# Kernel optimization log

Measured on AMD Instinct MI355X. Metric: run time of the kernel, lower is better.

## Reference

```python
import jax, jax.numpy as jnp
import numpy as np
import math

HEAD_SIZE = 64
WINDOW = 512  # sliding_window_size


def setup_inputs() -> dict:
    key = jax.random.key(0)
    k1, k2, k3, k4 = jax.random.split(key, 4)
    B, T, C = 4, 4096, 1024
    x = jax.random.normal(k1, (B, T, C), dtype=jnp.float32)
    # torch nn.Linear(C, head_size, bias=False) computes x @ W.T with W [hs, C];
    # we store the transposed [C, hs] layout so projection is x @ w.
    s = 1.0 / math.sqrt(C)
    w_key = jax.random.uniform(k2, (C, HEAD_SIZE), jnp.float32, -s, s)
    w_query = jax.random.uniform(k3, (C, HEAD_SIZE), jnp.float32, -s, s)
    w_value = jax.random.uniform(k4, (C, HEAD_SIZE), jnp.float32, -s, s)
    return {"x": x, "w_key": w_key, "w_query": w_query, "w_value": w_value}


def reference(x, w_key, w_query, w_value):
    # Non-cache path (use_cache=False): keys/values are the fresh projections,
    # q_start = k_start = 0, win_size = sliding_window_size.
    B, T, C = x.shape
    q = x @ w_query          # [B, T, hs]
    k = x @ w_key            # [B, T, hs]
    v = x @ w_value          # [B, T, hs]

    # attn_scores = q @ k^T  -> [B, T, T]
    scores = jnp.einsum('btd,bsd->bts', q, k)

    # Sliding-window causal mask: invalid where diff < 0 or diff >= window,
    # with diff = q_pos - k_pos.
    pos = jnp.arange(T)
    diff = pos[:, None] - pos[None, :]          # [T, T]
    mask_bool = (diff < 0) | (diff >= WINDOW)

    scale = math.sqrt(HEAD_SIZE)
    scores = jnp.where(mask_bool[None, :, :], -jnp.inf, scores)
    attn = jax.nn.softmax(scores / scale, axis=-1)  # dropout p=0.0 -> identity

    out = jnp.einsum('bts,bsd->btd', attn, v)   # [B, T, hs]
    return out
```

## Files before the change

kernel.cpp:

```cpp
#include <hip/hip_runtime.h>
#include <hip/hip_bf16.h>
#include <math.h>

#define BB 4
#define TT 4096
#define CC 1024
#define HS 64
#define WIN 512
#define NROW (BB*TT)

typedef float f32x4 __attribute__((ext_vector_type(4)));
typedef short bf16x8 __attribute__((ext_vector_type(8)));

#define MFMA16(a, b, c) __builtin_amdgcn_mfma_f32_16x16x32_bf16((a), (b), (c), 0, 0, 0)

#define GLOAD_LDS(gp, lp) __builtin_amdgcn_global_load_lds( \
    (const __attribute__((address_space(1))) void*)(gp), \
    (__attribute__((address_space(3))) void*)(lp), 16, 0, 0)

__device__ inline unsigned short f2b(float f) {
  union { __hip_bfloat16 h; unsigned short u; } v;
  v.h = __float2bfloat16(f);
  return v.u;
}

__global__ __launch_bounds__(256) void pack_w_kernel(
    const float* __restrict__ wq, const float* __restrict__ wk,
    const float* __restrict__ wv, unsigned short* __restrict__ wp)
{
  int t = blockIdx.x * 256 + threadIdx.x;
  int kg = t / 48;
  int nq = t % 48;
  int n0 = nq * 4;
  int m  = n0 >> 6;
  int c  = n0 & 63;
  const float* w = (m == 0) ? wq : (m == 1) ? wk : wv;
  float4 v = *(const float4*)&w[(size_t)kg * HS + c];
  int kt = kg >> 5;
  int hi = (kg >> 3) & 3;
  int j  = kg & 7;
  float vals[4] = {v.x, v.y, v.z, v.w};
  #pragma unroll
  for (int i = 0; i < 4; ++i) {
    int n  = n0 + i;
    int nb = n >> 4;
    int rl = n & 15;
    int lane = hi * 16 + rl;
    wp[((size_t)(kt * 12 + nb) * 64 + lane) * 8 + j] = f2b(vals[i]);
  }
}

__global__ __launch_bounds__(512) void proj_mfma_kernel(
    const float* __restrict__ x, const unsigned short* __restrict__ wp,
    unsigned short* __restrict__ q_ws, unsigned short* __restrict__ k_ws,
    unsigned short* __restrict__ vt_ws)
{
  __shared__ unsigned char lds[131072];
  unsigned char* const xb0 = lds;
  unsigned char* const xb1 = lds + 16384;
  unsigned char* const wb0 = lds + 32768;
  unsigned char* const wb1 = lds + 81920;

  const int tid = threadIdx.x;
  const int l   = tid & 63;
  const int wid = tid >> 6;
  const int cq  = wid & 3;
  const int rh  = wid >> 2;
  const int rl  = l & 15;
  const int hi  = l >> 4;
  const int r0  = blockIdx.x * 64;

  f32x4 acc[2][3];
  #pragma unroll
  for (int g = 0; g < 2; ++g)
    #pragma unroll
    for (int j = 0; j < 3; ++j) acc[g][j] = (f32x4){0.f, 0.f, 0.f, 0.f};

  f32x4 xr[2][2];

#define SXL(KS) { \
    _Pragma("unroll") \
    for (int it = 0; it < 2; ++it) { \
      int u = it * 512 + tid; \
      const float* gp = x + (size_t)(r0 + (u >> 4)) * CC + (KS) * 128 + (u & 15) * 8; \
      xr[it][0] = *(const f32x4*)gp; \
      xr[it][1] = *(const f32x4*)(gp + 4); \
    } }

#define XPACK(XB) { \
    _Pragma("unroll") \
    for (int it = 0; it < 2; ++it) { \
      int u = it * 512 + tid; \
      int row = u >> 4, seg = u & 15; \
      uint4 pk; \
      pk.x = (unsigned)f2b(xr[it][0][0]) | ((unsigned)f2b(xr[it][0][1]) << 16); \
      pk.y = (unsigned)f2b(xr[it][0][2]) | ((unsigned)f2b(xr[it][0][3]) << 16); \
      pk.z = (unsigned)f2b(xr[it][1][0]) | ((unsigned)f2b(xr[it][1][1]) << 16); \
      pk.w = (unsigned)f2b(xr[it][1][2]) | ((unsigned)f2b(xr[it][1][3]) << 16); \
      *(uint4*)((XB) + row * 256 + (((seg ^ (row & 7))) << 4)) = pk; \
    } }

#define SW(KS, WB) { \
    const unsigned short* wsrc = wp + (size_t)(KS) * 24576; \
    _Pragma("unroll") \
    for (int i = 0; i < 6; ++i) { \
      int s = i * 512 + tid; \
      GLOAD_LDS(wsrc + s * 8, (WB) + s * 16); \
    } }

#define COMP(XB, WB) { \
    _Pragma("unroll") \
    for (int kt = 0; kt < 4; ++kt) { \
      bf16x8 afr[2]; \
      _Pragma("unroll") \
      for (int g = 0; g < 2; ++g) { \
        int row = rh * 32 + g * 16 + rl; \
        int seg = kt * 4 + hi; \
        afr[g] = *(const bf16x8*)((XB) + row * 256 + ((seg ^ (row & 7)) << 4)); \
      } \
      _Pragma("unroll") \
      for (int j = 0; j < 3; ++j) { \
        bf16x8 wf = *(const bf16x8*)((WB) + ((kt * 12 + cq * 3 + j) * 64 + l) * 16); \
        acc[0][j] = MFMA16(afr[0], wf, acc[0][j]); \
        acc[1][j] = MFMA16(afr[1], wf, acc[1][j]); \
      } \
    } }

  SXL(0)
  SW(0, wb0)
  XPACK(xb0)
  __syncthreads();

  #pragma unroll
  for (int ks = 0; ks < 8; ++ks) {
    unsigned char* const xc = (ks & 1) ? xb1 : xb0;
    unsigned char* const wc = (ks & 1) ? wb1 : wb0;
    unsigned char* const xn = (ks & 1) ? xb0 : xb1;
    unsigned char* const wn = (ks & 1) ? wb0 : wb1;
    if (ks < 7) { SXL(ks + 1) SW(ks + 1, wn) }
    COMP(xc, wc)
    if (ks < 7) { XPACK(xn) }
    __syncthreads();
  }
#undef SXL
#undef XPACK
#undef SW
#undef COMP

  #pragma unroll
  for (int g = 0; g < 2; ++g) {
    int rb = r0 + rh * 32 + g * 16;
    #pragma unroll
    for (int j = 0; j < 3; ++j) {
      int nb = cq * 3 + j;
      if (nb < 8) {
        unsigned short* dst = (nb < 4) ? q_ws : k_ws;
        int c = (nb & 3) * 16 + rl;
        #pragma unroll
        for (int r = 0; r < 4; ++r) {
          int row = rb + hi * 4 + r;
          dst[(size_t)row * HS + c] = f2b(acc[g][j][r]);
        }
      } else {
        int ch   = rb >> 6;
        int key0 = (rb & 63) + hi * 4;
        int d = (nb - 8) * 16 + rl;
        unsigned u0 = (unsigned)f2b(acc[g][j][0]) | ((unsigned)f2b(acc[g][j][1]) << 16);
        unsigned u1 = (unsigned)f2b(acc[g][j][2]) | ((unsigned)f2b(acc[g][j][3]) << 16);
        uint2 uu; uu.x = u0; uu.y = u1;
        *(uint2*)(vt_ws + (size_t)ch * 4096 + d * 64 + key0) = uu;
      }
    }
  }
}

__global__ __launch_bounds__(256) void attn_mfma_kernel(
    const unsigned short* __restrict__ q_ws, const unsigned short* __restrict__ k_ws,
    const unsigned short* __restrict__ vt_ws,
    float* __restrict__ op_ws, float* __restrict__ ml_ws)
{
  __shared__ uint4 smem4[1600];
  unsigned char* smem = (unsigned char*)smem4;

  const int tid = threadIdx.x;
  const int l   = tid & 63;
  const int wid = tid >> 6;
  const int rl  = l & 15;
  const int hi  = l >> 4;
  const int split = blockIdx.x & 1;
  const int bq  = blockIdx.x >> 1;
  const int b   = bq >> 6;
  const int qt  = bq & 63;
  const int t0  = qt * 64;
  const int t0w = t0 + wid * 16;

  const unsigned short* qrow = q_ws + (size_t)(b * TT + t0w + rl) * HS;
  bf16x8 qb0 = *(const bf16x8*)(qrow + hi * 8);
  bf16x8 qb1 = *(const bf16x8*)(qrow + 32 + hi * 8);

  f32x4 oacc[4];
  #pragma unroll
  for (int i = 0; i < 4; ++i) oacc[i] = (f32x4){0.f, 0.f, 0.f, 0.f};
  float m_run = -INFINITY, l_run = 0.f;

  int s_lo = t0 - WIN; if (s_lo < 0) s_lo = 0;
  const int nch = (t0 + 64 - s_lo) >> 6;
  const int h   = nch >> 1;
  const int c_lo = split ? (s_lo + h * 64) : s_lo;
  const int c_hi = split ? (t0 + 64) : (s_lo + h * 64);

  unsigned char* pbase = smem + 16384 + wid * 2304 + rl * 144;

  for (int sc = c_lo; sc < c_hi; sc += 64) {
    __syncthreads();
    {
      const unsigned short* kg = k_ws + (size_t)(b * TT + sc) * HS;
      const unsigned short* vg = vt_ws + (size_t)((b * TT + sc) >> 6) * 4096;
      #pragma unroll
      for (int i = 0; i < 2; ++i) {
        int idx = tid + i * 256;
        int row = idx >> 3;
        int c16 = idx & 7;
        uint4 kv = *(const uint4*)(kg + row * 64 + c16 * 8);
        uint4 vv = *(const uint4*)(vg + row * 64 + c16 * 8);
        *(uint4*)(smem + row * 128 + ((c16 ^ (row & 7)) * 16)) = kv;
        *(uint4*)(smem + 8192 + row * 128 + ((c16 ^ (row & 7)) * 16)) = vv;
      }
    }
    __syncthreads();

    f32x4 sacc[4];
    #pragma unroll
    for (int i = 0; i < 4; ++i) sacc[i] = (f32x4){0.f, 0.f, 0.f, 0.f};
    #pragma unroll
    for (int kb = 0; kb < 4; ++kb) {
      int row = kb * 16 + rl;
      unsigned char* kr = smem + row * 128;
      bf16x8 k0 = *(const bf16x8*)(kr + (((hi) ^ (row & 7)) * 16));
      bf16x8 k1 = *(const bf16x8*)(kr + (((4 + hi) ^ (row & 7)) * 16));
      sacc[kb] = MFMA16(k0, qb0, sacc[kb]);
      sacc[kb] = MFMA16(k1, qb1, sacc[kb]);
    }

    const int tg = t0w + rl;
    float p[16];
    float tm = -INFINITY;
    bool full = (sc + 63 <= t0w) && (sc >= t0w - 496);
    #pragma unroll
    for (int kb = 0; kb < 4; ++kb)
      #pragma unroll
      for (int r = 0; r < 4; ++r) {
        float v = sacc[kb][r] * 0.125f;
        if (!full) {
          int key = sc + kb * 16 + hi * 4 + r;
          int diff = tg - key;
          v = (diff >= 0 && diff < WIN) ? v : -INFINITY;
        }
        p[kb * 4 + r] = v;
        tm = fmaxf(tm, v);
      }
    tm = fmaxf(tm, __shfl_xor(tm, 16));
    tm = fmaxf(tm, __shfl_xor(tm, 32));
    float m_new = fmaxf(m_run, tm);
    float fac  = (m_new == -INFINITY) ? 1.f : __expf(m_run - m_new);
    float msub = (m_new == -INFINITY) ? 0.f : m_new;
    float lsum = 0.f;
    #pragma unroll
    for (int i = 0; i < 16; ++i) { p[i] = __expf(p[i] - msub); lsum += p[i]; }
    lsum += __shfl_xor(lsum, 16);
    lsum += __shfl_xor(lsum, 32);
    l_run = l_run * fac + lsum;
    m_run = m_new;

    #pragma unroll
    for (int kb = 0; kb < 4; ++kb) {
      unsigned u0 = (unsigned)f2b(p[kb * 4 + 0]) | ((unsigned)f2b(p[kb * 4 + 1]) << 16);
      unsigned u1 = (unsigned)f2b(p[kb * 4 + 2]) | ((unsigned)f2b(p[kb * 4 + 3]) << 16);
      uint2 uu; uu.x = u0; uu.y = u1;
      *(uint2*)(pbase + kb * 32 + hi * 8) = uu;
    }

    #pragma unroll
    for (int r = 0; r < 4; ++r) {
      float fr = __shfl(fac, (l & 48) | (hi * 4 + r));
      oacc[0][r] *= fr; oacc[1][r] *= fr; oacc[2][r] *= fr; oacc[3][r] *= fr;
    }

    bf16x8 pa0 = *(const bf16x8*)(pbase + hi * 16);
    bf16x8 pa1 = *(const bf16x8*)(pbase + 64 + hi * 16);
    #pragma unroll
    for (int f = 0; f < 4; ++f) {
      int d = f * 16 + rl;
      unsigned char* vr = smem + 8192 + d * 128;
      bf16x8 v0 = *(const bf16x8*)(vr + (((hi) ^ (d & 7)) * 16));
      bf16x8 v1 = *(const bf16x8*)(vr + (((4 + hi) ^ (d & 7)) * 16));
      oacc[f] = MFMA16(pa0, v0, oacc[f]);
      oacc[f] = MFMA16(pa1, v1, oacc[f]);
    }
  }

  #pragma unroll
  for (int r = 0; r < 4; ++r) {
    size_t gq = (size_t)(b * TT + t0w + hi * 4 + r);
    #pragma unroll
    for (int f = 0; f < 4; ++f)
      op_ws[(gq * 2 + split) * HS + f * 16 + rl] = oacc[f][r];
  }
  if (hi == 0) {
    size_t gq = (size_t)(b * TT + t0w + rl);
    ml_ws[gq * 4 + split * 2 + 0] = m_run;
    ml_ws[gq * 4 + split * 2 + 1] = l_run;
  }
}

__global__ __launch_bounds__(256) void reduce_kernel(
    const float* __restrict__ op_ws, const float* __restrict__ ml_ws,
    float* __restrict__ out)
{
  int gid = blockIdx.x * 256 + threadIdx.x;
  int r  = gid >> 4;
  int c4 = (gid & 15) * 4;
  float4 mlv = *(const float4*)&ml_ws[(size_t)r * 4];
  float M  = fmaxf(mlv.x, mlv.z);
  float a0 = __expf(mlv.x - M);
  float a1 = __expf(mlv.z - M);
  float inv = 1.f / (a0 * mlv.y + a1 * mlv.w);
  f32x4 o0 = *(const f32x4*)&op_ws[((size_t)r * 2 + 0) * HS + c4];
  f32x4 o1 = *(const f32x4*)&op_ws[((size_t)r * 2 + 1) * HS + c4];
  f32x4 o;
  #pragma unroll
  for (int i = 0; i < 4; ++i) o[i] = (o0[i] * a0 + o1[i] * a1) * inv;
  *(f32x4*)&out[(size_t)r * HS + c4] = o;
}

extern "C" void kernel_launch(void* const* d_in, const int* in_sizes, int n_in,
                              void* d_out, int out_size, void* d_ws, size_t ws_size,
                              hipStream_t stream) {
  const float* x  = (const float*)d_in[0];
  const float* wk = (const float*)d_in[1];
  const float* wq = (const float*)d_in[2];
  const float* wv = (const float*)d_in[3];
  float* out = (float*)d_out;

  unsigned short* wp    = (unsigned short*)d_ws;
  unsigned short* q_ws  = wp + 196608;
  unsigned short* k_ws  = q_ws + (size_t)NROW * HS;
  unsigned short* vt_ws = k_ws + (size_t)NROW * HS;
  float* op_ws = (float*)(vt_ws + (size_t)NROW * HS);
  float* ml_ws = op_ws + (size_t)NROW * 2 * HS;

  pack_w_kernel<<<192, 256, 0, stream>>>(wq, wk, wv, wp);
  proj_mfma_kernel<<<NROW / 64, 512, 0, stream>>>(x, wp, q_ws, k_ws, vt_ws);
  attn_mfma_kernel<<<BB * (TT / 64) * 2, 256, 0, stream>>>(q_ws, k_ws, vt_ws, op_ws, ml_ws);
  reduce_kernel<<<NROW * HS / 4 / 256, 256, 0, stream>>>(op_ws, ml_ws, out);
}
```

Measured before the change: 41.76 us.

## Prepack x to bf16 MFMA fragment layout in a separate pass

Adds a prep kernel that converts x to bf16 and stores it in a per-tile MFMA fragment layout, fused with the weight packing. The projection kernel then loads x fragments straight into registers, uses a smaller double-buffered LDS for weights only, and remaps waves so each computes six column blocks over one 16-row group. This removes the in-kernel conversion and LDS staging of x, but adds an extra full read of fp32 x plus a write and reread of the bf16 copy. The packed x buffer reuses the attention partial-output workspace.

```diff
diff --git a/kernel.cpp b/kernel.cpp
--- a/kernel.cpp
+++ b/kernel.cpp
@@ -8,6 +8,7 @@
 #define HS 64
 #define WIN 512
 #define NROW (BB*TT)
+#define TILE_SH 65536
 
 typedef float f32x4 __attribute__((ext_vector_type(4)));
 typedef short bf16x8 __attribute__((ext_vector_type(8)));
@@ -24,152 +25,142 @@
   return v.u;
 }
 
-__global__ __launch_bounds__(256) void pack_w_kernel(
+__global__ __launch_bounds__(256) void prep_kernel(
+    const float* __restrict__ x,
     const float* __restrict__ wq, const float* __restrict__ wk,
-    const float* __restrict__ wv, unsigned short* __restrict__ wp)
+    const float* __restrict__ wv,
+    unsigned short* __restrict__ xpk, unsigned short* __restrict__ wp)
 {
-  int t = blockIdx.x * 256 + threadIdx.x;
-  int kg = t / 48;
-  int nq = t % 48;
-  int n0 = nq * 4;
-  int m  = n0 >> 6;
-  int c  = n0 & 63;
-  const float* w = (m == 0) ? wq : (m == 1) ? wk : wv;
-  float4 v = *(const float4*)&w[(size_t)kg * HS + c];
-  int kt = kg >> 5;
-  int hi = (kg >> 3) & 3;
-  int j  = kg & 7;
-  float vals[4] = {v.x, v.y, v.z, v.w};
-  #pragma unroll
-  for (int i = 0; i < 4; ++i) {
-    int n  = n0 + i;
-    int nb = n >> 4;
-    int rl = n & 15;
-    int lane = hi * 16 + rl;
-    wp[((size_t)(kt * 12 + nb) * 64 + lane) * 8 + j] = f2b(vals[i]);
+  int t0 = blockIdx.x * 256 + threadIdx.x;
+
+  if (t0 < 49152) {
+    int kg = t0 / 48;
+    int nq = t0 % 48;
+    int n0 = nq * 4;
+    int m  = n0 >> 6;
+    int c  = n0 & 63;
+    const float* w = (m == 0) ? wq : (m == 1) ? wk : wv;
+    float4 v = *(const float4*)&w[(size_t)kg * HS + c];
+    int kt = kg >> 5;
+    int hi = (kg >> 3) & 3;
+    int j  = kg & 7;
+    float vals[4] = {v.x, v.y, v.z, v.w};
+    #pragma unroll
+    for (int i = 0; i < 4; ++i) {
+      int n  = n0 + i;
+      int nb = n >> 4;
+      int rl = n & 15;
+      int lane = hi * 16 + rl;
+      wp[((size_t)(kt * 12 + nb) * 64 + lane) * 8 + j] = f2b(vals[i]);
+    }
+  }
+
+  const int total  = NROW * CC / 8;
+  const int stride = 2048 * 256;
+  #pragma unroll 1
+  for (int i = t0; i < total; i += stride) {
+    int row = i >> 7;
+    int k8  = i & 127;
+    const float* gp = x + (size_t)row * CC + k8 * 8;
+    f32x4 a0 = *(const f32x4*)gp;
+    f32x4 a1 = *(const f32x4*)(gp + 4);
+    uint4 pk;
+    pk.x = (unsigned)f2b(a0[0]) | ((unsigned)f2b(a0[1]) << 16);
+    pk.y = (unsigned)f2b(a0[2]) | ((unsigned)f2b(a0[3]) << 16);
+    pk.z = (unsigned)f2b(a1[0]) | ((unsigned)f2b(a1[1]) << 16);
+    pk.w = (unsigned)f2b(a1[2]) | ((unsigned)f2b(a1[3]) << 16);
+    int tile = row >> 6, rr = row & 63;
+    int rg = rr >> 4, rl = rr & 15;
+    int kt = k8 >> 2, hi = k8 & 3;
+    int l  = hi * 16 + rl;
+    *(uint4*)(xpk + (size_t)tile * TILE_SH + (kt * 4 + rg) * 512 + l * 8) = pk;
   }
 }
 
 __global__ __launch_bounds__(512) void proj_mfma_kernel(
-    const float* __restrict__ x, const unsigned short* __restrict__ wp,
+    const unsigned short* __restrict__ xpk, const unsigned short* __restrict__ wp,
     unsigned short* __restrict__ q_ws, unsigned short* __restrict__ k_ws,
     unsigned short* __restrict__ vt_ws)
 {
-  __shared__ unsigned char lds[131072];
-  unsigned char* const xb0 = lds;
-  unsigned char* const xb1 = lds + 16384;
-  unsigned char* const wb0 = lds + 32768;
-  unsigned char* const wb1 = lds + 81920;
+  __shared__ unsigned char wbuf[2][24576];
 
   const int tid = threadIdx.x;
   const int l   = tid & 63;
   const int wid = tid >> 6;
-  const int cq  = wid & 3;
-  const int rh  = wid >> 2;
+  const int rg  = wid & 3;
+  const int ch  = wid >> 2;
   const int rl  = l & 15;
   const int hi  = l >> 4;
   const int r0  = blockIdx.x * 64;
-
-  f32x4 acc[2][3];
-  #pragma unroll
-  for (int g = 0; g < 2; ++g)
-    #pragma unroll
-    for (int j = 0; j < 3; ++j) acc[g][j] = (f32x4){0.f, 0.f, 0.f, 0.f};
-
-  f32x4 xr[2][2];
-
-#define SXL(KS) { \
+  const unsigned short* xt = xpk + (size_t)blockIdx.x * TILE_SH;
+
+  f32x4 acc[6];
+  #pragma unroll
+  for (int j = 0; j < 6; ++j) acc[j] = (f32x4){0.f, 0.f, 0.f, 0.f};
+
+#define LX(KS, DST) { \
+    DST[0] = *(const bf16x8*)(xt + (((KS) * 2 + 0) * 4 + rg) * 512 + l * 8); \
+    DST[1] = *(const bf16x8*)(xt + (((KS) * 2 + 1) * 4 + rg) * 512 + l * 8); }
+
+#define SW(KS, WB) { \
+    const unsigned short* wsrc = wp + (size_t)(KS) * 12288; \
     _Pragma("unroll") \
-    for (int it = 0; it < 2; ++it) { \
-      int u = it * 512 + tid; \
-      const float* gp = x + (size_t)(r0 + (u >> 4)) * CC + (KS) * 128 + (u & 15) * 8; \
-      xr[it][0] = *(const f32x4*)gp; \
-      xr[it][1] = *(const f32x4*)(gp + 4); \
-    } }
-
-#define XPACK(XB) { \
-    _Pragma("unroll") \
-    for (int it = 0; it < 2; ++it) { \
-      int u = it * 512 + tid; \
-      int row = u >> 4, seg = u & 15; \
-      uint4 pk; \
-      pk.x = (unsigned)f2b(xr[it][0][0]) | ((unsigned)f2b(xr[it][0][1]) << 16); \
-      pk.y = (unsigned)f2b(xr[it][0][2]) | ((unsigned)f2b(xr[it][0][3]) << 16); \
-      pk.z = (unsigned)f2b(xr[it][1][0]) | ((unsigned)f2b(xr[it][1][1]) << 16); \
-      pk.w = (unsigned)f2b(xr[it][1][2]) | ((unsigned)f2b(xr[it][1][3]) << 16); \
-      *(uint4*)((XB) + row * 256 + (((seg ^ (row & 7))) << 4)) = pk; \
-    } }
-
-#define SW(KS, WB) { \
-    const unsigned short* wsrc = wp + (size_t)(KS) * 24576; \
-    _Pragma("unroll") \
-    for (int i = 0; i < 6; ++i) { \
+    for (int i = 0; i < 3; ++i) { \
       int s = i * 512 + tid; \
       GLOAD_LDS(wsrc + s * 8, (WB) + s * 16); \
     } }
 
-#define COMP(XB, WB) { \
+#define COMP(XF, WB) { \
     _Pragma("unroll") \
-    for (int kt = 0; kt < 4; ++kt) { \
-      bf16x8 afr[2]; \
+    for (int ktl = 0; ktl < 2; ++ktl) \
       _Pragma("unroll") \
-      for (int g = 0; g < 2; ++g) { \
-        int row = rh * 32 + g * 16 + rl; \
-        int seg = kt * 4 + hi; \
-        afr[g] = *(const bf16x8*)((XB) + row * 256 + ((seg ^ (row & 7)) << 4)); \
-      } \
-      _Pragma("unroll") \
-      for (int j = 0; j < 3; ++j) { \
-        bf16x8 wf = *(const bf16x8*)((WB) + ((kt * 12 + cq * 3 + j) * 64 + l) * 16); \
-        acc[0][j] = MFMA16(afr[0], wf, acc[0][j]); \
-        acc[1][j] = MFMA16(afr[1], wf, acc[1][j]); \
-      } \
-    } }
-
-  SXL(0)
-  SW(0, wb0)
-  XPACK(xb0)
+      for (int j = 0; j < 6; ++j) { \
+        bf16x8 wf = *(const bf16x8*)((WB) + ((ktl * 12 + ch * 6 + j) * 64 + l) * 16); \
+        acc[j] = MFMA16(XF[ktl], wf, acc[j]); \
+      } }
+
+  bf16x8 xA[2], xB[2];
+
+  LX(0, xA)
+  SW(0, wbuf[0])
+  LX(1, xB)
+  SW(1, wbuf[1])
   __syncthreads();
 
-  #pragma unroll
-  for (int ks = 0; ks < 8; ++ks) {
-    unsigned char* const xc = (ks & 1) ? xb1 : xb0;
-    unsigned char* const wc = (ks & 1) ? wb1 : wb0;
-    unsigned char* const xn = (ks & 1) ? xb0 : xb1;
-    unsigned char* const wn = (ks & 1) ? wb0 : wb1;
-    if (ks < 7) { SXL(ks + 1) SW(ks + 1, wn) }
-    COMP(xc, wc)
-    if (ks < 7) { XPACK(xn) }
+  #pragma unroll 1
+  for (int ks = 0; ks < 16; ks += 2) {
+    COMP(xA, wbuf[0])
+    if (ks + 2 < 16) { LX(ks + 2, xA) }
     __syncthreads();
-  }
-#undef SXL
-#undef XPACK
+    if (ks + 2 < 16) { SW(ks + 2, wbuf[0]) }
+    COMP(xB, wbuf[1])
+    if (ks + 3 < 16) { LX(ks + 3, xB) }
+    __syncthreads();
+    if (ks + 3 < 16) { SW(ks + 3, wbuf[1]) }
+  }
+#undef LX
 #undef SW
 #undef COMP
 
-  #pragma unroll
-  for (int g = 0; g < 2; ++g) {
-    int rb = r0 + rh * 32 + g * 16;
-    #pragma unroll
-    for (int j = 0; j < 3; ++j) {
-      int nb = cq * 3 + j;
-      if (nb < 8) {
-        unsigned short* dst = (nb < 4) ? q_ws : k_ws;
-        int c = (nb & 3) * 16 + rl;
-        #pragma unroll
-        for (int r = 0; r < 4; ++r) {
-          int row = rb + hi * 4 + r;
-          dst[(size_t)row * HS + c] = f2b(acc[g][j][r]);
-        }
-      } else {
-        int ch   = rb >> 6;
-        int key0 = (rb & 63) + hi * 4;
-        int d = (nb - 8) * 16 + rl;
-        unsigned u0 = (unsigned)f2b(acc[g][j][0]) | ((unsigned)f2b(acc[g][j][1]) << 16);
-        unsigned u1 = (unsigned)f2b(acc[g][j][2]) | ((unsigned)f2b(acc[g][j][3]) << 16);
-        uint2 uu; uu.x = u0; uu.y = u1;
-        *(uint2*)(vt_ws + (size_t)ch * 4096 + d * 64 + key0) = uu;
+  const int rb = r0 + rg * 16;
+  #pragma unroll
+  for (int j = 0; j < 6; ++j) {
+    int nb = ch * 6 + j;
+    if (nb < 8) {
+      unsigned short* dst = (nb < 4) ? q_ws : k_ws;
+      int c = (nb & 3) * 16 + rl;
+      #pragma unroll
+      for (int r = 0; r < 4; ++r) {
+        int row = rb + hi * 4 + r;
+        dst[(size_t)row * HS + c] = f2b(acc[j][r]);
       }
+    } else {
+      int key0 = rg * 16 + hi * 4;
+      int d = (nb - 8) * 16 + rl;
+      unsigned u0 = (unsigned)f2b(acc[j][0]) | ((unsigned)f2b(acc[j][1]) << 16);
+      unsigned u1 = (unsigned)f2b(acc[j][2]) | ((unsigned)f2b(acc[j][3]) << 16);
+      uint2 uu; uu.x = u0; uu.y = u1;
+      *(uint2*)(vt_ws + (size_t)blockIdx.x * 4096 + d * 64 + key0) = uu;
     }
   }
 }
@@ -346,11 +337,13 @@
   unsigned short* q_ws  = wp + 196608;
   unsigned short* k_ws  = q_ws + (size_t)NROW * HS;
   unsigned short* vt_ws = k_ws + (size_t)NROW * HS;
-  float* op_ws = (float*)(vt_ws + (size_t)NROW * HS);
+  unsigned short* shared_base = vt_ws + (size_t)NROW * HS;
+  unsigned short* xpk  = shared_base;
+  float* op_ws = (float*)shared_base;
   float* ml_ws = op_ws + (size_t)NROW * 2 * HS;
 
-  pack_w_kernel<<<192, 256, 0, stream>>>(wq, wk, wv, wp);
-  proj_mfma_kernel<<<NROW / 64, 512, 0, stream>>>(x, wp, q_ws, k_ws, vt_ws);
+  prep_kernel<<<2048, 256, 0, stream>>>(x, wq, wk, wv, xpk, wp);
+  proj_mfma_kernel<<<NROW / 64, 512, 0, stream>>>(xpk, wp, q_ws, k_ws, vt_ws);
   attn_mfma_kernel<<<BB * (TT / 64) * 2, 256, 0, stream>>>(q_ws, k_ws, vt_ws, op_ws, ml_ws);
   reduce_kernel<<<NROW * HS / 4 / 256, 256, 0, stream>>>(op_ws, ml_ws, out);
 }
```

Result: slower. 56.96 us (+36.4%).
